# Kernel optimization log

Hardware: AMD Instinct MI355X
Metric: run time of the kernel (lower is better)

Reference implementation:

```python
import jax, jax.numpy as jnp
import numpy as np

B, N, IN_FT, OUT_FT = 256, 512, 64, 64


def setup_inputs() -> dict:
    key = jax.random.key(0)
    k1, k2, k3 = jax.random.split(key, 3)
    seq = jax.random.normal(k1, (B, N, IN_FT), dtype=jnp.float32)
    adj = jax.random.uniform(k2, (B, N, N), dtype=jnp.float32)
    # Xavier-uniform linear weight [out_ft, in_ft]
    limit = float(np.sqrt(6.0 / (IN_FT + OUT_FT)))
    W = jax.random.uniform(k3, (OUT_FT, IN_FT), dtype=jnp.float32, minval=-limit, maxval=limit)
    bias = jnp.zeros((OUT_FT,), dtype=jnp.float32)  # bias.data.fill_(0.0)
    alpha = jnp.asarray(0.25, dtype=jnp.float32)    # PReLU default single param
    return {"seq": seq, "adj": adj, "W": W, "bias": bias, "alpha": alpha}


def reference(seq, adj, W, bias, alpha):
    # fc: seq @ W.T  -> [B, N, out_ft]
    seq_fts = jnp.einsum('bnf,of->bno', seq, W)
    # dense batched adjacency aggregation: adj @ seq_fts -> [B, N, out_ft]
    out = jnp.einsum('bnm,bmo->bno', adj, seq_fts)
    out = out + bias
    # PReLU with shared alpha
    return jnp.where(out >= 0, out, alpha * out)
```

## Files before the change

### kernel.cpp

```cpp
#include <hip/hip_runtime.h>
#include <hip/hip_bf16.h>


#define BATCH 256
#define NTOK  512
#define INF   64
#define OUTF  64

typedef __attribute__((ext_vector_type(8))) __bf16 bf16x8;
typedef __attribute__((ext_vector_type(4))) __bf16 bf16x4;
typedef __attribute__((ext_vector_type(4))) float  f32x4;

typedef const __attribute__((address_space(1))) char GChar;
typedef __attribute__((address_space(3))) char LChar;

__device__ __forceinline__ bf16x8 load_cvt8(const float* __restrict__ p) {
    float4 lo = *(const float4*)p;
    float4 hi = *(const float4*)(p + 4);
    bf16x8 r;
    r[0] = (__bf16)lo.x; r[1] = (__bf16)lo.y; r[2] = (__bf16)lo.z; r[3] = (__bf16)lo.w;
    r[4] = (__bf16)hi.x; r[5] = (__bf16)hi.y; r[6] = (__bf16)hi.z; r[7] = (__bf16)hi.w;
    return r;
}

__device__ __forceinline__ bf16x8 pack8(float4 lo, float4 hi) {
    bf16x8 r;
    r[0] = (__bf16)lo.x; r[1] = (__bf16)lo.y; r[2] = (__bf16)lo.z; r[3] = (__bf16)lo.w;
    r[4] = (__bf16)hi.x; r[5] = (__bf16)hi.y; r[6] = (__bf16)hi.z; r[7] = (__bf16)hi.w;
    return r;
}

__global__ __launch_bounds__(512, 2) void GCN_fused_kernel(
        const float* __restrict__ seq, const float* __restrict__ adj,
        const float* __restrict__ W, const float* __restrict__ bias,
        const float* __restrict__ alpha_p, float* __restrict__ out) {
    __shared__ float smem[32768];

    int b    = blockIdx.x;
    int tid  = threadIdx.x;
    int wave = tid >> 6;
    int lane = tid & 63;
    int row16 = lane & 15;
    int g     = lane >> 4;
    int mt    = wave >> 1;
    int c2    = wave & 1;
    int rs    = row16 & 7;

    __bf16* sft = (__bf16*)smem;
    float* buf0 = smem + 16384;
    float* buf1 = smem;

    const float* gadj = adj + (size_t)b * NTOK * NTOK;

#define STAGE(dstf, RG, KH) do {                                               \
    _Pragma("unroll")                                                          \
    for (int i_ = 0; i_ < 8; ++i_) {                                           \
        int idx_ = wave * 8 + i_;                                              \
        __builtin_amdgcn_global_load_lds(                                      \
            (GChar*)(gadj + (size_t)((RG) * 64 + idx_) * NTOK + (KH) * 256     \
                     + ((lane ^ (idx_ & 7)) << 2)),                            \
            (LChar*)((dstf) + idx_ * 256), 16, 0, 0);                          \
    }                                                                          \
} while (0)

    STAGE(buf0, 0, 0);
    __builtin_amdgcn_sched_barrier(0);

    {
        int mb = wave * 64;
        bf16x8 wf[4][2];
#pragma unroll
        for (int nt = 0; nt < 4; ++nt)
#pragma unroll
            for (int ks = 0; ks < 2; ++ks)
                wf[nt][ks] = load_cvt8(W + (size_t)(nt * 16 + row16) * INF + ks * 32 + g * 8);

#pragma unroll
        for (int mt2 = 0; mt2 < 4; ++mt2) {
            f32x4 pa[4] = {};
#pragma unroll
            for (int ks = 0; ks < 2; ++ks) {
                bf16x8 af = load_cvt8(seq + ((size_t)b * NTOK + mb + mt2 * 16 + row16) * INF + ks * 32 + g * 8);
#pragma unroll
                for (int nt = 0; nt < 4; ++nt)
                    pa[nt] = __builtin_amdgcn_mfma_f32_16x16x32_bf16(af, wf[nt][ks], pa[nt], 0, 0, 0);
            }
#pragma unroll
            for (int nt = 0; nt < 4; ++nt) {
                int o    = nt * 16 + row16;
                int ktok = mb + mt2 * 16 + g * 4;
                int sw   = (ktok >> 3) ^ (o & 7);
                bf16x4 v;
                v[0] = (__bf16)pa[nt][0]; v[1] = (__bf16)pa[nt][1];
                v[2] = (__bf16)pa[nt][2]; v[3] = (__bf16)pa[nt][3];
                *(bf16x4*)((char*)sft + (size_t)o * 1024 + sw * 16 + (ktok & 7) * 2) = v;
            }
        }
    }
    float bv2[2];
#pragma unroll
    for (int ti = 0; ti < 2; ++ti) bv2[ti] = bias[c2 * 32 + ti * 16 + row16];
    float alphav = alpha_p[0];
    __syncthreads();

    bf16x8 bbr2[16][2];
#pragma unroll
    for (int t = 0; t < 16; ++t)
#pragma unroll
        for (int ti = 0; ti < 2; ++ti) {
            int o  = c2 * 32 + ti * 16 + row16;
            int sw = ((t << 2) + g) ^ rs;
            bbr2[t][ti] = *(const bf16x8*)((const char*)sft + (size_t)o * 1024 + sw * 16);
        }
    __syncthreads();

    f32x4 acc2[2];
#pragma unroll
    for (int ti = 0; ti < 2; ++ti) {
        acc2[ti][0] = bv2[ti]; acc2[ti][1] = bv2[ti];
        acc2[ti][2] = bv2[ti]; acc2[ti][3] = bv2[ti];
    }

#define COMPUTE(curf, KH) do {                                                 \
    int rowb_ = (mt * 16 + row16) * 256;                                       \
    _Pragma("unroll")                                                          \
    for (int tt_ = 0; tt_ < 8; ++tt_) {                                        \
        int s0_ = ((tt_ * 8 + g * 2) ^ rs);                                    \
        float4 f0_ = *(const float4*)((curf) + rowb_ + s0_ * 4);               \
        float4 f1_ = *(const float4*)((curf) + rowb_ + (s0_ ^ 1) * 4);         \
        bf16x8 a_ = pack8(f0_, f1_);                                           \
        acc2[0] = __builtin_amdgcn_mfma_f32_16x16x32_bf16(a_, bbr2[(KH) * 8 + tt_][0], acc2[0], 0, 0, 0); \
        acc2[1] = __builtin_amdgcn_mfma_f32_16x16x32_bf16(a_, bbr2[(KH) * 8 + tt_][1], acc2[1], 0, 0, 0); \
    }                                                                          \
} while (0)

#pragma unroll 1
    for (int rg = 0; rg < 8; ++rg) {
        if (rg > 0) {
            __builtin_amdgcn_sched_barrier(0);
            __builtin_amdgcn_s_barrier();
            __builtin_amdgcn_sched_barrier(0);
        }
        STAGE(buf1, rg, 1);
        __builtin_amdgcn_sched_barrier(0);
        if (rg == 0) asm volatile("s_waitcnt vmcnt(8)"  ::: "memory");
        else         asm volatile("s_waitcnt vmcnt(12)" ::: "memory");
        __builtin_amdgcn_sched_barrier(0);
        __builtin_amdgcn_s_barrier();
        __builtin_amdgcn_sched_barrier(0);
        COMPUTE(buf0, 0);

        __builtin_amdgcn_sched_barrier(0);
        __builtin_amdgcn_s_barrier();
        __builtin_amdgcn_sched_barrier(0);
        if (rg < 7) STAGE(buf0, rg + 1, 0);
        __builtin_amdgcn_sched_barrier(0);
        if (rg < 7) asm volatile("s_waitcnt vmcnt(8)" ::: "memory");
        else        asm volatile("s_waitcnt vmcnt(0)" ::: "memory");
        __builtin_amdgcn_sched_barrier(0);
        __builtin_amdgcn_s_barrier();
        __builtin_amdgcn_sched_barrier(0);
        COMPUTE(buf1, 1);

        {
            float p0[4], p1[4];
#pragma unroll
            for (int j = 0; j < 4; ++j) {
                float v0 = acc2[0][j]; p0[j] = (v0 >= 0.f) ? v0 : alphav * v0;
                float v1 = acc2[1][j]; p1[j] = (v1 >= 0.f) ? v1 : alphav * v1;
            }
            int addrA = (g * 16 + ((2 * row16) & 15)) << 2;
            int addrB = (g * 16 + ((2 * row16 + 1) & 15)) << 2;
            bool loSel = (row16 < 8);
#pragma unroll
            for (int j = 0; j < 4; ++j) {
                int a0 = __builtin_amdgcn_ds_bpermute(addrA, __float_as_int(p0[j]));
                int a1 = __builtin_amdgcn_ds_bpermute(addrA, __float_as_int(p1[j]));
                int b0 = __builtin_amdgcn_ds_bpermute(addrB, __float_as_int(p0[j]));
                int b1 = __builtin_amdgcn_ds_bpermute(addrB, __float_as_int(p1[j]));
                float lo = __int_as_float(loSel ? a0 : a1);
                float hi = __int_as_float(loSel ? b0 : b1);
                float2 st = make_float2(lo, hi);
                *(float2*)(out + ((size_t)b * NTOK + rg * 64 + mt * 16 + g * 4 + j) * OUTF
                           + c2 * 32 + 2 * row16) = st;
                acc2[0][j] = bv2[0];
                acc2[1][j] = bv2[1];
            }
        }
    }
#undef STAGE
#undef COMPUTE
}

extern "C" void kernel_launch(void* const* d_in, const int* in_sizes, int n_in,
                              void* d_out, int out_size, void* d_ws, size_t ws_size,
                              hipStream_t stream) {
    const float* seq   = (const float*)d_in[0];
    const float* adj   = (const float*)d_in[1];
    const float* W     = (const float*)d_in[2];
    const float* bias  = (const float*)d_in[3];
    const float* alpha = (const float*)d_in[4];
    float* out = (float*)d_out;

    GCN_fused_kernel<<<dim3(BATCH), dim3(512), 0, stream>>>(seq, adj, W, bias, alpha, out);
}
```

Baseline: 68.66 us.

## Switch adjacency staging to four-buffer 32KB chunk pipeline with one barrier per chunk

Replaces the two 64KB half-row-group buffers with four 32KB quarter-chunks, prefetching two chunks ahead so each step needs one barrier instead of two. Bias and alpha loads are hoisted before the first staging, and the __syncthreads calls become explicit lgkmcnt waits plus raw barriers. Launch bounds drop the min-2-blocks hint, giving the compiler more register freedom but possibly lowering occupancy. The aim is to keep more global loads in flight and cut barrier stalls, at the cost of finer-grained chunks and more vmcnt bookkeeping.

```diff
diff --git a/kernel.cpp b/kernel.cpp
--- a/kernel.cpp
+++ b/kernel.cpp
@@ -30,7 +30,7 @@
     return r;
 }
 
-__global__ __launch_bounds__(512, 2) void GCN_fused_kernel(
+__global__ __launch_bounds__(512) void GCN_fused_kernel(
         const float* __restrict__ seq, const float* __restrict__ adj,
         const float* __restrict__ W, const float* __restrict__ bias,
         const float* __restrict__ alpha_p, float* __restrict__ out) {
@@ -46,24 +46,34 @@
     int c2    = wave & 1;
     int rs    = row16 & 7;
 
-    __bf16* sft = (__bf16*)smem;
-    float* buf0 = smem + 16384;
-    float* buf1 = smem;
+    __bf16* sft  = (__bf16*)smem;
+    float* bufp2 = smem;
+    float* bufp3 = smem + 8192;
+    float* bufp0 = smem + 16384;
+    float* bufp1 = smem + 24576;
 
     const float* gadj = adj + (size_t)b * NTOK * NTOK;
 
-#define STAGE(dstf, RG, KH) do {                                               \
+#define STAGE(dstf, CH) do {                                                   \
     _Pragma("unroll")                                                          \
-    for (int i_ = 0; i_ < 8; ++i_) {                                           \
-        int idx_ = wave * 8 + i_;                                              \
+    for (int i_ = 0; i_ < 4; ++i_) {                                           \
+        int idx_ = wave * 4 + i_;                                              \
+        int rl_  = 2 * idx_ + (lane >> 5);                                     \
+        int sl_  = (lane & 31) ^ (rl_ & 7);                                    \
         __builtin_amdgcn_global_load_lds(                                      \
-            (GChar*)(gadj + (size_t)((RG) * 64 + idx_) * NTOK + (KH) * 256     \
-                     + ((lane ^ (idx_ & 7)) << 2)),                            \
+            (GChar*)(gadj + (size_t)(((CH) >> 2) * 64 + rl_) * NTOK            \
+                     + ((CH) & 3) * 128 + sl_ * 4),                            \
             (LChar*)((dstf) + idx_ * 256), 16, 0, 0);                          \
     }                                                                          \
 } while (0)
 
-    STAGE(buf0, 0, 0);
+    float bv2[2];
+#pragma unroll
+    for (int ti = 0; ti < 2; ++ti) bv2[ti] = bias[c2 * 32 + ti * 16 + row16];
+    float alphav = alpha_p[0];
+
+    STAGE(bufp0, 0);
+    STAGE(bufp1, 1);
     __builtin_amdgcn_sched_barrier(0);
 
     {
@@ -97,11 +107,10 @@
             }
         }
     }
-    float bv2[2];
-#pragma unroll
-    for (int ti = 0; ti < 2; ++ti) bv2[ti] = bias[c2 * 32 + ti * 16 + row16];
-    float alphav = alpha_p[0];
-    __syncthreads();
+    asm volatile("s_waitcnt lgkmcnt(0)" ::: "memory");
+    __builtin_amdgcn_sched_barrier(0);
+    __builtin_amdgcn_s_barrier();
+    __builtin_amdgcn_sched_barrier(0);
 
     bf16x8 bbr2[16][2];
 #pragma unroll
@@ -112,7 +121,10 @@
             int sw = ((t << 2) + g) ^ rs;
             bbr2[t][ti] = *(const bf16x8*)((const char*)sft + (size_t)o * 1024 + sw * 16);
         }
-    __syncthreads();
+    asm volatile("s_waitcnt lgkmcnt(0)" ::: "memory");
+    __builtin_amdgcn_sched_barrier(0);
+    __builtin_amdgcn_s_barrier();
+    __builtin_amdgcn_sched_barrier(0);
 
     f32x4 acc2[2];
 #pragma unroll
@@ -121,75 +133,66 @@
         acc2[ti][2] = bv2[ti]; acc2[ti][3] = bv2[ti];
     }
 
-#define COMPUTE(curf, KH) do {                                                 \
-    int rowb_ = (mt * 16 + row16) * 256;                                       \
-    _Pragma("unroll")                                                          \
-    for (int tt_ = 0; tt_ < 8; ++tt_) {                                        \
-        int s0_ = ((tt_ * 8 + g * 2) ^ rs);                                    \
-        float4 f0_ = *(const float4*)((curf) + rowb_ + s0_ * 4);               \
-        float4 f1_ = *(const float4*)((curf) + rowb_ + (s0_ ^ 1) * 4);         \
-        bf16x8 a_ = pack8(f0_, f1_);                                           \
-        acc2[0] = __builtin_amdgcn_mfma_f32_16x16x32_bf16(a_, bbr2[(KH) * 8 + tt_][0], acc2[0], 0, 0, 0); \
-        acc2[1] = __builtin_amdgcn_mfma_f32_16x16x32_bf16(a_, bbr2[(KH) * 8 + tt_][1], acc2[1], 0, 0, 0); \
-    }                                                                          \
-} while (0)
-
 #pragma unroll 1
     for (int rg = 0; rg < 8; ++rg) {
-        if (rg > 0) {
+#pragma unroll
+        for (int kq = 0; kq < 4; ++kq) {
+            float* cur = (kq == 0) ? bufp0 : (kq == 1) ? bufp1
+                       : (kq == 2) ? bufp2 : bufp3;
+            float* nxt = (kq == 0) ? bufp2 : (kq == 1) ? bufp3
+                       : (kq == 2) ? bufp0 : bufp1;
+
+            if (rg == 0 && kq == 0)      asm volatile("s_waitcnt vmcnt(4)" ::: "memory");
+            else if (rg == 7 && kq == 3) asm volatile("s_waitcnt vmcnt(0)" ::: "memory");
+            else if (kq == 0)            asm volatile("s_waitcnt vmcnt(8)" ::: "memory");
+            else                         asm volatile("s_waitcnt vmcnt(4)" ::: "memory");
             __builtin_amdgcn_sched_barrier(0);
             __builtin_amdgcn_s_barrier();
             __builtin_amdgcn_sched_barrier(0);
-        }
-        STAGE(buf1, rg, 1);
-        __builtin_amdgcn_sched_barrier(0);
-        if (rg == 0) asm volatile("s_waitcnt vmcnt(8)"  ::: "memory");
-        else         asm volatile("s_waitcnt vmcnt(12)" ::: "memory");
-        __builtin_amdgcn_sched_barrier(0);
-        __builtin_amdgcn_s_barrier();
-        __builtin_amdgcn_sched_barrier(0);
-        COMPUTE(buf0, 0);
-
-        __builtin_amdgcn_sched_barrier(0);
-        __builtin_amdgcn_s_barrier();
-        __builtin_amdgcn_sched_barrier(0);
-        if (rg < 7) STAGE(buf0, rg + 1, 0);
-        __builtin_amdgcn_sched_barrier(0);
-        if (rg < 7) asm volatile("s_waitcnt vmcnt(8)" ::: "memory");
-        else        asm volatile("s_waitcnt vmcnt(0)" ::: "memory");
-        __builtin_amdgcn_sched_barrier(0);
-        __builtin_amdgcn_s_barrier();
-        __builtin_amdgcn_sched_barrier(0);
-        COMPUTE(buf1, 1);
-
-        {
-            float p0[4], p1[4];
-#pragma unroll
-            for (int j = 0; j < 4; ++j) {
-                float v0 = acc2[0][j]; p0[j] = (v0 >= 0.f) ? v0 : alphav * v0;
-                float v1 = acc2[1][j]; p1[j] = (v1 >= 0.f) ? v1 : alphav * v1;
-            }
-            int addrA = (g * 16 + ((2 * row16) & 15)) << 2;
-            int addrB = (g * 16 + ((2 * row16 + 1) & 15)) << 2;
-            bool loSel = (row16 < 8);
-#pragma unroll
-            for (int j = 0; j < 4; ++j) {
-                int a0 = __builtin_amdgcn_ds_bpermute(addrA, __float_as_int(p0[j]));
-                int a1 = __builtin_amdgcn_ds_bpermute(addrA, __float_as_int(p1[j]));
-                int b0 = __builtin_amdgcn_ds_bpermute(addrB, __float_as_int(p0[j]));
-                int b1 = __builtin_amdgcn_ds_bpermute(addrB, __float_as_int(p1[j]));
-                float lo = __int_as_float(loSel ? a0 : a1);
-                float hi = __int_as_float(loSel ? b0 : b1);
-                float2 st = make_float2(lo, hi);
-                *(float2*)(out + ((size_t)b * NTOK + rg * 64 + mt * 16 + g * 4 + j) * OUTF
-                           + c2 * 32 + 2 * row16) = st;
-                acc2[0][j] = bv2[0];
-                acc2[1][j] = bv2[1];
+            if (!(rg == 7 && kq >= 2)) STAGE(nxt, rg * 4 + kq + 2);
+            __builtin_amdgcn_sched_barrier(0);
+
+            {
+                int rowb_ = (mt * 16 + row16) * 128;
+#pragma unroll
+                for (int tt = 0; tt < 4; ++tt) {
+                    int s0 = (tt * 8 + g * 2) ^ rs;
+                    float4 f0 = *(const float4*)(cur + rowb_ + s0 * 4);
+                    float4 f1 = *(const float4*)(cur + rowb_ + (s0 ^ 1) * 4);
+                    bf16x8 a = pack8(f0, f1);
+                    acc2[0] = __builtin_amdgcn_mfma_f32_16x16x32_bf16(a, bbr2[kq * 4 + tt][0], acc2[0], 0, 0, 0);
+                    acc2[1] = __builtin_amdgcn_mfma_f32_16x16x32_bf16(a, bbr2[kq * 4 + tt][1], acc2[1], 0, 0, 0);
+                }
+            }
+
+            if (kq == 3) {
+                float p0[4], p1[4];
+#pragma unroll
+                for (int j = 0; j < 4; ++j) {
+                    float v0 = acc2[0][j]; p0[j] = (v0 >= 0.f) ? v0 : alphav * v0;
+                    float v1 = acc2[1][j]; p1[j] = (v1 >= 0.f) ? v1 : alphav * v1;
+                }
+                int addrA = (g * 16 + ((2 * row16) & 15)) << 2;
+                int addrB = (g * 16 + ((2 * row16 + 1) & 15)) << 2;
+                bool loSel = (row16 < 8);
+#pragma unroll
+                for (int j = 0; j < 4; ++j) {
+                    int a0 = __builtin_amdgcn_ds_bpermute(addrA, __float_as_int(p0[j]));
+                    int a1 = __builtin_amdgcn_ds_bpermute(addrA, __float_as_int(p1[j]));
+                    int b0 = __builtin_amdgcn_ds_bpermute(addrB, __float_as_int(p0[j]));
+                    int b1 = __builtin_amdgcn_ds_bpermute(addrB, __float_as_int(p1[j]));
+                    float lo = __int_as_float(loSel ? a0 : a1);
+                    float hi = __int_as_float(loSel ? b0 : b1);
+                    float2 st = make_float2(lo, hi);
+                    *(float2*)(out + ((size_t)b * NTOK + rg * 64 + mt * 16 + g * 4 + j) * OUTF
+                               + c2 * 32 + 2 * row16) = st;
+                    acc2[0][j] = bv2[0];
+                    acc2[1][j] = bv2[1];
+                }
             }
         }
     }
 #undef STAGE
-#undef COMPUTE
 }
 
 extern "C" void kernel_launch(void* const* d_in, const int* in_sizes, int n_in,
```

New measurement: 69.50 us. No clear change (+1.2%).
